# Kernel optimization log

Measured on AMD Instinct MI355X. Metric: run time of the kernel, lower is better.

Reference implementation:

```python
import jax, jax.numpy as jnp
import numpy as np

BN_EPS = 1e-3  # keras BatchNormalization default


def _bn(x, gamma, beta, mean, var):
    # inference-mode batchnorm over channel (last) axis
    return (x - mean) * (gamma * jax.lax.rsqrt(var + BN_EPS)) + beta


def _rel_pos_idx(n):
    # replicate calc_rel_pos: pos (n*n, 2); rel = pos[None]-pos[:,None] + n-1
    ii, jj = np.meshgrid(np.arange(n), np.arange(n), indexing='ij')
    pos = np.stack([ii.reshape(-1), jj.reshape(-1)], axis=-1)  # (n*n, 2)
    rel = pos[None, :, :] - pos[:, None, :] + (n - 1)          # (n*n, n*n, 2)
    return jnp.asarray(rel, dtype=jnp.int32)


def setup_inputs() -> dict:
    key = jax.random.key(0)
    ks = jax.random.split(key, 13)
    b, hh, ww, c = 4, 16, 16, 1024
    heads, dim_k, dim_u, dim_out = 4, 256, 1, 1024
    dim_v = dim_out // heads  # 256 == dim_k (required by the original reshape)
    n = hh
    rel_len = 2 * n - 1
    inp = {
        'x': jax.random.normal(ks[0], (b, hh, ww, c), jnp.float32),
        'Wq': jax.random.normal(ks[1], (c, dim_k * heads), jnp.float32) * 0.02,
        'Wk': jax.random.normal(ks[2], (c, dim_k * dim_u), jnp.float32) * 0.02,
        'Wv': jax.random.normal(ks[3], (c, dim_v * dim_u), jnp.float32) * 0.02,
        'q_gamma': jax.random.normal(ks[4], (dim_k * heads,), jnp.float32),
        'q_beta': jax.random.normal(ks[5], (dim_k * heads,), jnp.float32),
        'q_mean': jax.random.normal(ks[6], (dim_k * heads,), jnp.float32),
        'q_var': jax.random.uniform(ks[7], (dim_k * heads,), jnp.float32, 0.5, 1.5),
        'v_gamma': jax.random.normal(ks[8], (dim_v * dim_u,), jnp.float32),
        'v_beta': jax.random.normal(ks[9], (dim_v * dim_u,), jnp.float32),
        'v_mean': jax.random.normal(ks[10], (dim_v * dim_u,), jnp.float32),
        'v_var': jax.random.uniform(ks[11], (dim_v * dim_u,), jnp.float32, 0.5, 1.5),
        'rel_pos_emb': jax.random.normal(ks[12], (rel_len, rel_len, dim_k, dim_u), jnp.float32) * 0.05,
    }
    return inp


def reference(x, Wq, Wk, Wv, q_gamma, q_beta, q_mean, q_var,
              v_gamma, v_beta, v_mean, v_var, rel_pos_emb):
    b, hh, ww, c = x.shape
    heads, dim_u = 4, 1
    dim_k = rel_pos_emb.shape[2]
    dim_v = Wv.shape[1] // dim_u
    m = hh * ww

    # 1x1 conv projections (no bias)
    q = jnp.einsum('bhwc,cd->bhwd', x, Wq)
    k = jnp.einsum('bhwc,cd->bhwd', x, Wk)
    v = jnp.einsum('bhwc,cd->bhwd', x, Wv)

    q = _bn(q, q_gamma, q_beta, q_mean, q_var)
    v = _bn(v, v_gamma, v_beta, v_mean, v_var)

    # faithful TF row-major reshapes (note: mixes spatial/channel exactly as original)
    q = q.reshape(b, heads, dim_v, m)   # (b, h, k, n)
    k = k.reshape(b, dim_u, dim_v, m)   # (b, u, k, m)
    v = v.reshape(b, dim_u, dim_v, m)   # (b, u, v, m)

    k = jax.nn.softmax(k, axis=-1)

    Lc = jnp.einsum('bukm,buvm->bkv', k, v)
    Yc = jnp.einsum('bhkn,bkv->bnhv', q, Lc)

    rel_pos = _rel_pos_idx(hh)  # (m, m, 2) int32 constants
    rel = rel_pos_emb[rel_pos[..., 0], rel_pos[..., 1]]  # (m, m, k, u)
    Lp = jnp.einsum('nmku,buvm->bnkv', rel, v)
    Yp = jnp.einsum('bhkn,bnkv->bnhv', q, Lp)

    Y = Yc + Yp  # (b, n, h, v)
    return Y.reshape(b, hh, ww, heads * dim_v)
```

## Files before the change

kernel.cpp:

```cpp
#include <hip/hip_runtime.h>


typedef __bf16 bf16;
typedef __attribute__((ext_vector_type(8))) __bf16 bf16x8;
typedef __attribute__((ext_vector_type(4))) float f32x4;

__device__ __forceinline__ bf16x8 ld8(const bf16* p) {
    return *reinterpret_cast<const bf16x8*>(p);
}

__global__ __launch_bounds__(256) void prep(
    const float* __restrict__ x, const float* __restrict__ Wq,
    const float* __restrict__ Wk, const float* __restrict__ Wv,
    const float* __restrict__ rpe, bf16* __restrict__ xb,
    bf16* __restrict__ WqT, bf16* __restrict__ WkT, bf16* __restrict__ WvT,
    bf16* __restrict__ rpeb) {
    __shared__ float tile[32][33];
    const int bid = blockIdx.x, tid = threadIdx.x;
    const float* W = nullptr;
    bf16* WT = nullptr;
    int ldw = 0, ci = 0, di = 0;
    if (bid < 1024) {
        W = Wq; WT = WqT; ldw = 1024; ci = bid >> 5; di = bid & 31;
    } else if (bid < 1280) {
        const int t2 = bid - 1024;
        W = Wk; WT = WkT; ldw = 256; ci = t2 >> 3; di = t2 & 7;
    } else if (bid < 1536) {
        const int t2 = bid - 1280;
        W = Wv; WT = WvT; ldw = 256; ci = t2 >> 3; di = t2 & 7;
    }
    if (W) {
        const int r = tid >> 3, c4 = (tid & 7) * 4;
        const float4 v =
            *reinterpret_cast<const float4*>(&W[(ci * 32 + r) * ldw + di * 32 + c4]);
        tile[r][c4 + 0] = v.x;
        tile[r][c4 + 1] = v.y;
        tile[r][c4 + 2] = v.z;
        tile[r][c4 + 3] = v.w;
        __syncthreads();
        bf16* dst = &WT[(di * 32 + r) * 1024 + ci * 32 + c4];
        dst[0] = (bf16)tile[c4 + 0][r];
        dst[1] = (bf16)tile[c4 + 1][r];
        dst[2] = (bf16)tile[c4 + 2][r];
        dst[3] = (bf16)tile[c4 + 3][r];
        return;
    }
    if (bid < 1792) {
        const int base = (bid - 1536) * 1024 + tid;
        const float4* xs = reinterpret_cast<const float4*>(x);
#pragma unroll
        for (int j = 0; j < 4; ++j) {
            const float4 v = xs[base + j * 256];
            bf16* d = &xb[(base + j * 256) * 4];
            d[0] = (bf16)v.x; d[1] = (bf16)v.y; d[2] = (bf16)v.z; d[3] = (bf16)v.w;
        }
        return;
    }
    {
        const int base = (bid - 1792) * 1024 + tid;
        const float4* rs = reinterpret_cast<const float4*>(rpe);
#pragma unroll
        for (int j = 0; j < 4; ++j) {
            const int idx = base + j * 256;
            if (idx < 61504) {
                const float4 v = rs[idx];
                bf16* d = &rpeb[idx * 4];
                d[0] = (bf16)v.x; d[1] = (bf16)v.y; d[2] = (bf16)v.z; d[3] = (bf16)v.w;
            }
        }
    }
}

template <int PA, int PB>
__device__ __forceinline__ void kpass(const bf16* __restrict__ Ap, int offA,
                                      const bf16* __restrict__ Bp,
                                      bf16* __restrict__ Al, bf16* __restrict__ Bl,
                                      f32x4 (&acc)[2][2], int m0, int n0,
                                      int nsteps) {
    const int tid = threadIdx.x;
    const int w = tid >> 6, l = tid & 63;
    const int sr0 = tid >> 3, sg = tid & 7;
    const int wr = (w >> 1) * 32, wc = (w & 1) * 32;
    const int fr = l & 15, fk = (l >> 4) * 8;
    const int st0 = sr0 * 64 + ((sg ^ (sr0 & 7)) << 3);
    const int st1 = (sr0 + 32) * 64 + ((sg ^ (sr0 & 7)) << 3);
    const int fx = (fr & 7) << 3;
    const bf16* arow0 = Ap + (m0 + sr0) * PA + offA + sg * 8;
    const bf16* arow1 = Ap + (m0 + 32 + sr0) * PA + offA + sg * 8;
    const bf16* brow0 = Bp + (n0 + sr0) * PB + sg * 8;
    const bf16* brow1 = Bp + (n0 + 32 + sr0) * PB + sg * 8;
    bf16x8 a0 = ld8(arow0), a1 = ld8(arow1), b0 = ld8(brow0), b1 = ld8(brow1);
    for (int kt = 0; kt < nsteps; ++kt) {
        __syncthreads();
        *reinterpret_cast<bf16x8*>(&Al[st0]) = a0;
        *reinterpret_cast<bf16x8*>(&Al[st1]) = a1;
        *reinterpret_cast<bf16x8*>(&Bl[st0]) = b0;
        *reinterpret_cast<bf16x8*>(&Bl[st1]) = b1;
        __syncthreads();
        if (kt + 1 < nsteps) {
            const int k0 = (kt + 1) * 64;
            a0 = ld8(arow0 + k0);
            a1 = ld8(arow1 + k0);
            b0 = ld8(brow0 + k0);
            b1 = ld8(brow1 + k0);
        }
#pragma unroll
        for (int ks = 0; ks < 2; ++ks) {
            const int eo = (ks * 32 + fk) ^ fx;
            const bf16x8 af0 = ld8(&Al[(wr + fr) * 64 + eo]);
            const bf16x8 af1 = ld8(&Al[(wr + 16 + fr) * 64 + eo]);
            const bf16x8 bg0 = ld8(&Bl[(wc + fr) * 64 + eo]);
            const bf16x8 bg1 = ld8(&Bl[(wc + 16 + fr) * 64 + eo]);
            acc[0][0] = __builtin_amdgcn_mfma_f32_16x16x32_bf16(af0, bg0, acc[0][0], 0, 0, 0);
            acc[0][1] = __builtin_amdgcn_mfma_f32_16x16x32_bf16(af0, bg1, acc[0][1], 0, 0, 0);
            acc[1][0] = __builtin_amdgcn_mfma_f32_16x16x32_bf16(af1, bg0, acc[1][0], 0, 0, 0);
            acc[1][1] = __builtin_amdgcn_mfma_f32_16x16x32_bf16(af1, bg1, acc[1][1], 0, 0, 0);
        }
    }
}

__global__ __launch_bounds__(256) void proj_all(
    const bf16* __restrict__ xb, const bf16* __restrict__ WqT,
    const bf16* __restrict__ WkT, const bf16* __restrict__ WvT,
    const float* __restrict__ qg, const float* __restrict__ qb,
    const float* __restrict__ qm, const float* __restrict__ qv,
    const float* __restrict__ vg, const float* __restrict__ vb,
    const float* __restrict__ vm, const float* __restrict__ vvar,
    bf16* __restrict__ Q2, float* __restrict__ kn, bf16* __restrict__ vbn) {
    const int z = blockIdx.z;
    const int m0 = blockIdx.y * 64;
    const int tid = threadIdx.x;
    const int w = tid >> 6, l = tid & 63;
    int n0, mode;
    const bf16* Bg;
    if (z < 4) { mode = 0; Bg = WqT; n0 = (z * 4 + blockIdx.x) * 64; }
    else if (z == 4) { mode = 1; Bg = WkT; n0 = blockIdx.x * 64; }
    else { mode = 2; Bg = WvT; n0 = blockIdx.x * 64; }
    __shared__ __align__(16) bf16 Al[4096];
    __shared__ __align__(16) bf16 Bl[4096];
    f32x4 acc[2][2] = {};
    kpass<1024, 1024>(xb, 0, Bg, Al, Bl, acc, m0, n0, 16);

    const int wr = (w >> 1) * 32, wc = (w & 1) * 32;
    const int drow = (l >> 4) * 4, dcol = l & 15;
#pragma unroll
    for (int ms = 0; ms < 2; ++ms) {
#pragma unroll
        for (int ns = 0; ns < 2; ++ns) {
            const int gc = n0 + wc + ns * 16 + dcol;
            float scale = 1.f, shift = 0.f;
            if (mode == 0) {
                scale = qg[gc] * rsqrtf(qv[gc] + 1e-3f);
                shift = qb[gc] - qm[gc] * scale;
            } else if (mode == 2) {
                scale = vg[gc] * rsqrtf(vvar[gc] + 1e-3f);
                shift = vb[gc] - vm[gc] * scale;
            }
#pragma unroll
            for (int r = 0; r < 4; ++r) {
                const int gr = m0 + wr + ms * 16 + drow + r;
                const float val = acc[ms][ns][r] * scale + shift;
                if (mode == 0) {
                    const int bh = gr >> 6;
                    const int kk = (gr & 63) * 4 + (gc >> 8);
                    Q2[bh * 65536 + (gc & 255) * 256 + kk] = (bf16)val;
                } else if (mode == 1) {
                    kn[gr * 256 + gc] = val;
                } else {
                    vbn[gr * 256 + gc] = (bf16)val;
                }
            }
        }
    }
}

__global__ __launch_bounds__(256) void lc_s(
    const float* __restrict__ kn, const bf16* __restrict__ vbn,
    const bf16* __restrict__ rpeb, const bf16* __restrict__ Q2,
    bf16* __restrict__ LcT, bf16* __restrict__ S) {
    __shared__ __align__(16) bf16 smem[20480];
    const int tid = threadIdx.x;
    const int w = tid >> 6, l = tid & 63;
    const int fr = l & 15, fk = (l >> 4) * 8;
    const int fx = (fr & 7) << 3;

    if (blockIdx.y < 16) {
        const int b = blockIdx.y >> 2;
        const int m0v = (blockIdx.y & 3) * 64;
        const int n0k = blockIdx.x * 64;
        bf16* Bfull = smem;
        bf16* Al = smem + 16384;

        const float* knb = kn + (b * 256 + n0k) * 256;
        const int row = tid >> 2, cq = (tid & 3) * 4;
        const float* src = knb + row * 256;
        float mx = -3.4e38f;
#pragma unroll
        for (int i = 0; i < 16; ++i) {
            const float4 v = *reinterpret_cast<const float4*>(&src[cq + i * 16]);
            mx = fmaxf(fmaxf(fmaxf(v.x, v.y), fmaxf(v.z, v.w)), mx);
        }
        mx = fmaxf(mx, __shfl_xor(mx, 1));
        mx = fmaxf(mx, __shfl_xor(mx, 2));
        float sum = 0.f;
#pragma unroll
        for (int i = 0; i < 16; ++i) {
            const float4 v = *reinterpret_cast<const float4*>(&src[cq + i * 16]);
            sum += expf(v.x - mx) + expf(v.y - mx) + expf(v.z - mx) + expf(v.w - mx);
        }
        sum += __shfl_xor(sum, 1);
        sum += __shfl_xor(sum, 2);
        const float inv = 1.f / sum;
#pragma unroll
        for (int i = 0; i < 16; ++i) {
            const int col = cq + i * 16;
            const float4 v = *reinterpret_cast<const float4*>(&src[col]);
            bf16 o[4] = {(bf16)(expf(v.x - mx) * inv), (bf16)(expf(v.y - mx) * inv),
                         (bf16)(expf(v.z - mx) * inv), (bf16)(expf(v.w - mx) * inv)};
            const int elem =
                row * 256 + ((((col >> 3) ^ (row & 7)) << 3) | (col & 7));
            *reinterpret_cast<uint2*>(&Bfull[elem]) = *reinterpret_cast<uint2*>(o);
        }

        const int sr0 = tid >> 3, sg = tid & 7;
        const int st0 = sr0 * 64 + ((sg ^ (sr0 & 7)) << 3);
        const int st1 = (sr0 + 32) * 64 + ((sg ^ (sr0 & 7)) << 3);
        const int wr = (w >> 1) * 32, wc = (w & 1) * 32;
        const bf16* va0 = vbn + (b * 256 + m0v + sr0) * 256 + sg * 8;
        const bf16* va1 = va0 + 32 * 256;
        bf16x8 a0 = ld8(va0), a1 = ld8(va1);
        f32x4 acc[2][2] = {};
        for (int kt = 0; kt < 4; ++kt) {
            __syncthreads();
            *reinterpret_cast<bf16x8*>(&Al[st0]) = a0;
            *reinterpret_cast<bf16x8*>(&Al[st1]) = a1;
            __syncthreads();
            if (kt + 1 < 4) {
                a0 = ld8(va0 + (kt + 1) * 64);
                a1 = ld8(va1 + (kt + 1) * 64);
            }
#pragma unroll
            for (int ks = 0; ks < 2; ++ks) {
                const int eoA = (ks * 32 + fk) ^ fx;
                const int kg = kt * 64 + ks * 32 + fk;
                const int eoB = kg ^ fx;
                const bf16x8 af0 = ld8(&Al[(wr + fr) * 64 + eoA]);
                const bf16x8 af1 = ld8(&Al[(wr + 16 + fr) * 64 + eoA]);
                const bf16x8 bg0 = ld8(&Bfull[(wc + fr) * 256 + eoB]);
                const bf16x8 bg1 = ld8(&Bfull[(wc + 16 + fr) * 256 + eoB]);
                acc[0][0] = __builtin_amdgcn_mfma_f32_16x16x32_bf16(af0, bg0, acc[0][0], 0, 0, 0);
                acc[0][1] = __builtin_amdgcn_mfma_f32_16x16x32_bf16(af0, bg1, acc[0][1], 0, 0, 0);
                acc[1][0] = __builtin_amdgcn_mfma_f32_16x16x32_bf16(af1, bg0, acc[1][0], 0, 0, 0);
                acc[1][1] = __builtin_amdgcn_mfma_f32_16x16x32_bf16(af1, bg1, acc[1][1], 0, 0, 0);
            }
        }
        const int drow = (l >> 4) * 4, dcol = l & 15;
#pragma unroll
        for (int ms = 0; ms < 2; ++ms)
#pragma unroll
            for (int ns = 0; ns < 2; ++ns)
#pragma unroll
                for (int r = 0; r < 4; ++r)
                    LcT[b * 65536 + (m0v + wr + ms * 16 + drow + r) * 256 + n0k +
                        wc + ns * 16 + dcol] = (bf16)acc[ms][ns][r];
        return;
    }

    const int n = blockIdx.y - 16;
    const int m0 = blockIdx.x * 64;
    const int in_ = n >> 4, jn = n & 15;
    bf16* Als = smem;
    bf16* Bls = smem + 16384;
#pragma unroll
    for (int i = 0; i < 2; ++i) {
        const int slot = tid + i * 256;
        const int row = slot >> 5, g = slot & 31;
        *reinterpret_cast<bf16x8*>(&Bls[row * 256 + ((g ^ (row & 7)) << 3)]) =
            ld8(Q2 + row * 65536 + n * 256 + g * 8);
    }
#pragma unroll
    for (int i = 0; i < 8; ++i) {
        const int slot = tid + i * 256;
        const int row = slot >> 5, g = slot & 31;
        const int m = m0 + row;
        const int ridx = ((m >> 4) - in_ + 15) * 31 + ((m & 15) - jn + 15);
        *reinterpret_cast<bf16x8*>(&Als[row * 256 + ((g ^ (row & 7)) << 3)]) =
            ld8(rpeb + ridx * 256 + g * 8);
    }
    __syncthreads();
    f32x4 acc = {};
#pragma unroll
    for (int ks = 0; ks < 8; ++ks) {
        const int eo = (ks * 32 + fk) ^ fx;
        const bf16x8 af = ld8(&Als[(w * 16 + fr) * 256 + eo]);
        const bf16x8 bg = ld8(&Bls[fr * 256 + eo]);
        acc = __builtin_amdgcn_mfma_f32_16x16x32_bf16(af, bg, acc, 0, 0, 0);
    }
    const int drow = (l >> 4) * 4, bh = l & 15;
#pragma unroll
    for (int r = 0; r < 4; ++r) {
        const int m = m0 + w * 16 + drow + r;
        S[n * 4096 + bh * 256 + m] = (bf16)acc[r];
    }
}

__global__ __launch_bounds__(256) void yfinal(const bf16* __restrict__ Q2,
                                              const bf16* __restrict__ LcT,
                                              float* __restrict__ out,
                                              const bf16* __restrict__ S,
                                              const bf16* __restrict__ vbn) {
    const int tid = threadIdx.x;
    const int w = tid >> 6, l = tid & 63;
    const int m0 = blockIdx.y * 64, n0 = blockIdx.x * 64;
    const int z = blockIdx.z;
    __shared__ __align__(16) bf16 Al[4096];
    __shared__ __align__(16) bf16 Bl[4096];
    f32x4 acc[2][2] = {};
    kpass<256, 256>(Q2 + z * 65536, 0, LcT + (z >> 2) * 65536, Al, Bl, acc, m0, n0, 4);
    kpass<4096, 256>(S, z * 256, vbn + (z >> 2) * 65536, Al, Bl, acc, m0, n0, 4);

    const int wr = (w >> 1) * 32, wc = (w & 1) * 32;
    const int drow = (l >> 4) * 4, dcol = l & 15;
#pragma unroll
    for (int ms = 0; ms < 2; ++ms)
#pragma unroll
        for (int ns = 0; ns < 2; ++ns)
#pragma unroll
            for (int r = 0; r < 4; ++r)
                out[(z >> 2) * 262144 + (m0 + wr + ms * 16 + drow + r) * 1024 +
                    (z & 3) * 256 + n0 + wc + ns * 16 + dcol] = acc[ms][ns][r];
}

extern "C" void kernel_launch(void* const* d_in, const int* in_sizes, int n_in,
                              void* d_out, int out_size, void* d_ws, size_t ws_size,
                              hipStream_t stream) {
    const float* x = (const float*)d_in[0];
    const float* Wq = (const float*)d_in[1];
    const float* Wk = (const float*)d_in[2];
    const float* Wv = (const float*)d_in[3];
    const float* qg = (const float*)d_in[4];
    const float* qb = (const float*)d_in[5];
    const float* qm = (const float*)d_in[6];
    const float* qv = (const float*)d_in[7];
    const float* vg = (const float*)d_in[8];
    const float* vb = (const float*)d_in[9];
    const float* vm = (const float*)d_in[10];
    const float* vvar = (const float*)d_in[11];
    const float* rpe = (const float*)d_in[12];
    float* out = (float*)d_out;

    char* wsb = (char*)d_ws;
    bf16* xb = (bf16*)(wsb);
    bf16* WqT = (bf16*)(wsb + 0x200000u);
    bf16* WkT = (bf16*)(wsb + 0x400000u);
    bf16* WvT = (bf16*)(wsb + 0x480000u);
    bf16* rpeb = (bf16*)(wsb + 0x500000u);
    bf16* Q2 = (bf16*)(wsb + 0x580000u);
    bf16* vbn = (bf16*)(wsb + 0x800000u);
    bf16* LcT = (bf16*)(wsb + 0x880000u);
    bf16* S = (bf16*)(wsb + 0x900000u);
    float* kn = (float*)(wsb + 0xB00000u);

    const dim3 blk(256);
    prep<<<1853, blk, 0, stream>>>(x, Wq, Wk, Wv, rpe, xb, WqT, WkT, WvT, rpeb);
    proj_all<<<dim3(4, 16, 6), blk, 0, stream>>>(xb, WqT, WkT, WvT, qg, qb, qm, qv,
                                                 vg, vb, vm, vvar, Q2, kn, vbn);
    lc_s<<<dim3(4, 272), blk, 0, stream>>>(kn, vbn, rpeb, Q2, LcT, S);
    yfinal<<<dim3(4, 4, 16), blk, 0, stream>>>(Q2, LcT, out, S, vbn);
}
```

Measured before the change: 43.08 us.

## Use direct global-to-LDS loads with double-buffered GEMM pipeline

Replaces the register-staged global→LDS copy in the GEMM k-loop with global_load_lds direct transfers into a double-buffered shared tile. The next tile is fetched while MFMAs run on the current one, which cuts one barrier per step and the register round-trip. The rel-pos gather kernel also switches to direct LDS loads, with the swizzle applied on the source address. LDS use doubles, and correctness depends on the per-lane LDS layout the builtin produces matching the swizzled read pattern.

```diff
diff --git a/kernel.cpp b/kernel.cpp
--- a/kernel.cpp
+++ b/kernel.cpp
@@ -7,6 +7,12 @@
 
 __device__ __forceinline__ bf16x8 ld8(const bf16* p) {
     return *reinterpret_cast<const bf16x8*>(p);
+}
+
+__device__ __forceinline__ void gload16(const void* g, void* l) {
+    __builtin_amdgcn_global_load_lds(
+        (const __attribute__((address_space(1))) void*)g,
+        (__attribute__((address_space(3))) void*)l, 16, 0, 0);
 }
 
 __global__ __launch_bounds__(256) void prep(
@@ -72,38 +78,41 @@
 }
 
 template <int PA, int PB>
-__device__ __forceinline__ void kpass(const bf16* __restrict__ Ap, int offA,
-                                      const bf16* __restrict__ Bp,
-                                      bf16* __restrict__ Al, bf16* __restrict__ Bl,
-                                      f32x4 (&acc)[2][2], int m0, int n0,
-                                      int nsteps) {
+__device__ __forceinline__ void kpass2(const bf16* __restrict__ Ap, int offA,
+                                       const bf16* __restrict__ Bp,
+                                       bf16* __restrict__ AlB, bf16* __restrict__ BlB,
+                                       f32x4 (&acc)[2][2], int m0, int n0,
+                                       int nsteps) {
     const int tid = threadIdx.x;
     const int w = tid >> 6, l = tid & 63;
-    const int sr0 = tid >> 3, sg = tid & 7;
     const int wr = (w >> 1) * 32, wc = (w & 1) * 32;
     const int fr = l & 15, fk = (l >> 4) * 8;
-    const int st0 = sr0 * 64 + ((sg ^ (sr0 & 7)) << 3);
-    const int st1 = (sr0 + 32) * 64 + ((sg ^ (sr0 & 7)) << 3);
     const int fx = (fr & 7) << 3;
-    const bf16* arow0 = Ap + (m0 + sr0) * PA + offA + sg * 8;
-    const bf16* arow1 = Ap + (m0 + 32 + sr0) * PA + offA + sg * 8;
-    const bf16* brow0 = Bp + (n0 + sr0) * PB + sg * 8;
-    const bf16* brow1 = Bp + (n0 + 32 + sr0) * PB + sg * 8;
-    bf16x8 a0 = ld8(arow0), a1 = ld8(arow1), b0 = ld8(brow0), b1 = ld8(brow1);
+    const int srow = l >> 3;
+    const int sgr = (l & 7) ^ srow;
+    const bf16* asrc = Ap + (m0 + w * 16 + srow) * PA + offA + sgr * 8;
+    const bf16* bsrc = Bp + (n0 + w * 16 + srow) * PB + sgr * 8;
+    const int ldst = (w * 16) * 64;
+
+    int buf = 0;
+    {
+        gload16(asrc, AlB + ldst);
+        gload16(asrc + 8 * PA, AlB + ldst + 8 * 64);
+        gload16(bsrc, BlB + ldst);
+        gload16(bsrc + 8 * PB, BlB + ldst + 8 * 64);
+    }
+    __syncthreads();
     for (int kt = 0; kt < nsteps; ++kt) {
-        __syncthreads();
-        *reinterpret_cast<bf16x8*>(&Al[st0]) = a0;
-        *reinterpret_cast<bf16x8*>(&Al[st1]) = a1;
-        *reinterpret_cast<bf16x8*>(&Bl[st0]) = b0;
-        *reinterpret_cast<bf16x8*>(&Bl[st1]) = b1;
-        __syncthreads();
         if (kt + 1 < nsteps) {
             const int k0 = (kt + 1) * 64;
-            a0 = ld8(arow0 + k0);
-            a1 = ld8(arow1 + k0);
-            b0 = ld8(brow0 + k0);
-            b1 = ld8(brow1 + k0);
-        }
+            const int d2 = (buf ^ 1) * 4096 + ldst;
+            gload16(asrc + k0, AlB + d2);
+            gload16(asrc + 8 * PA + k0, AlB + d2 + 8 * 64);
+            gload16(bsrc + k0, BlB + d2);
+            gload16(bsrc + 8 * PB + k0, BlB + d2 + 8 * 64);
+        }
+        const bf16* Al = AlB + buf * 4096;
+        const bf16* Bl = BlB + buf * 4096;
 #pragma unroll
         for (int ks = 0; ks < 2; ++ks) {
             const int eo = (ks * 32 + fk) ^ fx;
@@ -116,6 +125,8 @@
             acc[1][0] = __builtin_amdgcn_mfma_f32_16x16x32_bf16(af1, bg0, acc[1][0], 0, 0, 0);
             acc[1][1] = __builtin_amdgcn_mfma_f32_16x16x32_bf16(af1, bg1, acc[1][1], 0, 0, 0);
         }
+        __syncthreads();
+        buf ^= 1;
     }
 }
 
@@ -136,10 +147,10 @@
     if (z < 4) { mode = 0; Bg = WqT; n0 = (z * 4 + blockIdx.x) * 64; }
     else if (z == 4) { mode = 1; Bg = WkT; n0 = blockIdx.x * 64; }
     else { mode = 2; Bg = WvT; n0 = blockIdx.x * 64; }
-    __shared__ __align__(16) bf16 Al[4096];
-    __shared__ __align__(16) bf16 Bl[4096];
+    __shared__ __align__(16) bf16 Al[2][4096];
+    __shared__ __align__(16) bf16 Bl[2][4096];
     f32x4 acc[2][2] = {};
-    kpass<1024, 1024>(xb, 0, Bg, Al, Bl, acc, m0, n0, 16);
+    kpass2<1024, 1024>(xb, 0, Bg, &Al[0][0], &Bl[0][0], acc, m0, n0, 16);
 
     const int wr = (w >> 1) * 32, wc = (w & 1) * 32;
     const int drow = (l >> 4) * 4, dcol = l & 15;
@@ -242,8 +253,7 @@
 #pragma unroll
             for (int ks = 0; ks < 2; ++ks) {
                 const int eoA = (ks * 32 + fk) ^ fx;
-                const int kg = kt * 64 + ks * 32 + fk;
-                const int eoB = kg ^ fx;
+                const int eoB = (kt * 64 + ks * 32 + fk) ^ fx;
                 const bf16x8 af0 = ld8(&Al[(wr + fr) * 64 + eoA]);
                 const bf16x8 af1 = ld8(&Al[(wr + 16 + fr) * 64 + eoA]);
                 const bf16x8 bg0 = ld8(&Bfull[(wc + fr) * 256 + eoB]);
@@ -271,21 +281,23 @@
     const int in_ = n >> 4, jn = n & 15;
     bf16* Als = smem;
     bf16* Bls = smem + 16384;
-#pragma unroll
-    for (int i = 0; i < 2; ++i) {
-        const int slot = tid + i * 256;
-        const int row = slot >> 5, g = slot & 31;
-        *reinterpret_cast<bf16x8*>(&Bls[row * 256 + ((g ^ (row & 7)) << 3)]) =
-            ld8(Q2 + row * 65536 + n * 256 + g * 8);
-    }
-#pragma unroll
-    for (int i = 0; i < 8; ++i) {
-        const int slot = tid + i * 256;
-        const int row = slot >> 5, g = slot & 31;
-        const int m = m0 + row;
-        const int ridx = ((m >> 4) - in_ + 15) * 31 + ((m & 15) - jn + 15);
-        *reinterpret_cast<bf16x8*>(&Als[row * 256 + ((g ^ (row & 7)) << 3)]) =
-            ld8(rpeb + ridx * 256 + g * 8);
+    {
+        const int rp = l >> 5;
+        const int gsw = l & 31;
+#pragma unroll
+        for (int j = 0; j < 8; ++j) {
+            const int rrow = w * 16 + j * 2 + rp;
+            const int m = m0 + rrow;
+            const int ridx = ((m >> 4) - in_ + 15) * 31 + ((m & 15) - jn + 15);
+            gload16(rpeb + ridx * 256 + ((gsw ^ (rrow & 7)) << 3),
+                    Als + (w * 16 + j * 2) * 256);
+        }
+#pragma unroll
+        for (int j = 0; j < 2; ++j) {
+            const int rrow = w * 4 + j * 2 + rp;
+            gload16(Q2 + rrow * 65536 + n * 256 + ((gsw ^ (rrow & 7)) << 3),
+                    Bls + (w * 4 + j * 2) * 256);
+        }
     }
     __syncthreads();
     f32x4 acc = {};
@@ -313,11 +325,13 @@
     const int w = tid >> 6, l = tid & 63;
     const int m0 = blockIdx.y * 64, n0 = blockIdx.x * 64;
     const int z = blockIdx.z;
-    __shared__ __align__(16) bf16 Al[4096];
-    __shared__ __align__(16) bf16 Bl[4096];
+    __shared__ __align__(16) bf16 Al[2][4096];
+    __shared__ __align__(16) bf16 Bl[2][4096];
     f32x4 acc[2][2] = {};
-    kpass<256, 256>(Q2 + z * 65536, 0, LcT + (z >> 2) * 65536, Al, Bl, acc, m0, n0, 4);
-    kpass<4096, 256>(S, z * 256, vbn + (z >> 2) * 65536, Al, Bl, acc, m0, n0, 4);
+    kpass2<256, 256>(Q2 + z * 65536, 0, LcT + (z >> 2) * 65536, &Al[0][0], &Bl[0][0],
+                     acc, m0, n0, 4);
+    kpass2<4096, 256>(S, z * 256, vbn + (z >> 2) * 65536, &Al[0][0], &Bl[0][0],
+                      acc, m0, n0, 4);
 
     const int wr = (w >> 1) * 32, wc = (w & 1) * 32;
     const int drow = (l >> 4) * 4, dcol = l & 15;
```

Result: slower. 48.51 us (+12.6%).
